# Kernel optimization log

Hardware: AMD Instinct MI355X
Metric: run time of the kernel (lower is better)

Reference implementation:

```python
import jax, jax.numpy as jnp
import numpy as np

N_NODES = 50000
E_DIM = 128
H_DIM = 256
OUT_DIM = 2
N_EDGES = 800000
NEG_SLOPE = 0.01  # nn.LeakyReLU default


def gcn_conv(x, W, b, src, dst, n):
    """PyG GCNConv: h = x @ W; add self-loops; sym-normalized scatter-add; + bias."""
    h = x @ W  # [N, H]
    loop = jnp.arange(n, dtype=src.dtype)
    s = jnp.concatenate([src, loop])
    d = jnp.concatenate([dst, loop])
    w = jnp.ones_like(s, dtype=h.dtype)
    deg = jax.ops.segment_sum(w, d, num_segments=n)  # in-degree incl. self-loop
    dis = jnp.where(deg > 0, jax.lax.rsqrt(deg), jnp.zeros_like(deg))
    norm = dis[s] * dis[d]  # [E+N]
    msg = h[s] * norm[:, None]  # gather + scale
    out = jax.ops.segment_sum(msg, d, num_segments=n)  # scatter-add to targets
    return out + b


def setup_inputs() -> dict:
    key = jax.random.key(0)
    ks = jax.random.split(key, 12)
    inp = {
        "mask_feature": jax.random.normal(ks[0], (N_NODES, E_DIM), jnp.float32),
        "feature": jax.random.normal(ks[1], (N_NODES, E_DIM), jnp.float32),
        "edge_index": jax.random.randint(ks[2], (2, N_EDGES), 0, N_NODES, jnp.int64 if jax.config.jax_enable_x64 else jnp.int32),
        "edge_type": jax.random.randint(ks[3], (N_EDGES,), 0, 2, jnp.int64 if jax.config.jax_enable_x64 else jnp.int32),
        # learned parameters
        "W_in": jax.random.normal(ks[4], (E_DIM, H_DIM), jnp.float32) * 0.05,
        "b_in": jnp.zeros((H_DIM,), jnp.float32),
        "Wg1": jax.random.normal(ks[5], (H_DIM, H_DIM), jnp.float32) * 0.05,
        "bg1": jnp.zeros((H_DIM,), jnp.float32),
        "Wg2": jax.random.normal(ks[6], (H_DIM, H_DIM), jnp.float32) * 0.05,
        "bg2": jnp.zeros((H_DIM,), jnp.float32),
        "W_out": jax.random.normal(ks[7], (H_DIM, OUT_DIM), jnp.float32) * 0.05,
        "b_out": jnp.zeros((OUT_DIM,), jnp.float32),
    }
    return inp


def reference(mask_feature, feature, edge_index, edge_type,
              W_in, b_in, Wg1, bg1, Wg2, bg2, W_out, b_out):
    src, dst = edge_index[0], edge_index[1]
    n = mask_feature.shape[0]
    # main branch
    x = jax.nn.leaky_relu(mask_feature @ W_in + b_in, NEG_SLOPE)
    x = gcn_conv(x, Wg1, bg1, src, dst, n)
    # dropout is identity at inference
    x = gcn_conv(x, Wg2, bg2, src, dst, n)
    x = x @ W_out + b_out  # [N, out_dim]
    # mask branch
    m = jax.nn.leaky_relu((feature - mask_feature) @ W_in + b_in, NEG_SLOPE)
    m = m @ W_out + b_out  # [N, out_dim]
    return x * m
```

## Files before the change

kernel.cpp:

```cpp
#include <hip/hip_runtime.h>


#define NEG_SLOPE 0.01f
constexpr int HD = 256;
constexpr int CHUNK = 4096;
constexpr int BSTRIDE = 8192;

typedef __bf16 bf16x8 __attribute__((ext_vector_type(8)));
typedef unsigned short u16x8 __attribute__((ext_vector_type(8)));
typedef float f32x4 __attribute__((ext_vector_type(4)));

#define MFMA16 __builtin_amdgcn_mfma_f32_16x16x32_bf16

__device__ inline void split1(float v, unsigned short& h, unsigned short& l) {
  unsigned u = __float_as_uint(v);
  unsigned hb = u & 0xFFFF0000u;
  float lf = v - __uint_as_float(hb);
  unsigned ul = __float_as_uint(lf);
  h = (unsigned short)(hb >> 16);
  l = (unsigned short)((ul + 0x7FFFu + ((ul >> 16) & 1u)) >> 16);
}

__device__ inline unsigned short bf16rne(float v) {
  unsigned u = __float_as_uint(v);
  return (unsigned short)((u + 0x7FFFu + ((u >> 16) & 1u)) >> 16);
}

__global__ __launch_bounds__(256) void k_prep(
    const float* __restrict__ Win, u16x8* __restrict__ Wf,
    const float* __restrict__ Wg1, const float* __restrict__ Wg2,
    const float* __restrict__ Wo, const float* __restrict__ bin,
    const float* __restrict__ bg1, const float* __restrict__ bg2,
    const float* __restrict__ bo, float4* __restrict__ E1,
    float2* __restrict__ E2, float* __restrict__ uv, int* __restrict__ cur) {
  __shared__ float wt[256][2];
  const int bid = blockIdx.x, tid = threadIdx.x;
  if (bid < 16) {
    int f = bid * 4 + (tid >> 6);
    int lane = tid & 63;
    int nt = f >> 2, ks = f & 3;
    int n = nt * 16 + (lane & 15);
    int k0 = ks * 32 + (lane >> 4) * 8;
    u16x8 outv;
    #pragma unroll
    for (int j = 0; j < 8; ++j)
      outv[j] = bf16rne(Win[(size_t)(k0 + j) * HD + n]);
    Wf[f * 64 + lane] = outv;
  } else if (bid == 16) {
    int r = tid;
    float s0 = 0.f, s1 = 0.f;
    for (int k = 0; k < 256; ++k) {
      float w = Wg2[r * 256 + k];
      s0 = fmaf(w, Wo[k * 2 + 0], s0);
      s1 = fmaf(w, Wo[k * 2 + 1], s1);
    }
    wt[r][0] = s0; wt[r][1] = s1;
    __syncthreads();
    float b0 = 0.f, b1 = 0.f;
    for (int k = 0; k < 256; ++k) {
      float w = Wg1[r * 256 + k];
      b0 = fmaf(w, wt[k][0], b0);
      b1 = fmaf(w, wt[k][1], b1);
    }
    E1[r] = make_float4(bin[r], b0, b1, 0.f);
    E2[r] = make_float2(Wo[r * 2 + 0], Wo[r * 2 + 1]);
    if (r < 2) {
      float u = 0.f, v = 0.f;
      for (int k = 0; k < 256; ++k) {
        u = fmaf(bg1[k], wt[k][r], u);
        v = fmaf(bg2[k], Wo[k * 2 + r], v);
      }
      uv[r] = u;
      uv[2 + r] = v + bo[r];
    }
  } else {
    cur[tid] = 0;
  }
}

__global__ __launch_bounds__(256) void k_scatter(
    const int* __restrict__ src, const int* __restrict__ dst,
    int* __restrict__ cur, unsigned* __restrict__ packed, int E) {
  __shared__ int bins[256], lstart[256], gbase[256], lcur[256];
  __shared__ int wsum[4];
  __shared__ unsigned sbuf[CHUNK];
  const int t = threadIdx.x, b = blockIdx.x;
  const int lane = t & 63, wid = t >> 6;
  bins[t] = 0;
  __syncthreads();
  const int e0 = b * CHUNK, e1 = min(e0 + CHUNK, E), m = e1 - e0;
  for (int e = e0 + t; e < e1; e += 256)
    atomicAdd(&bins[dst[e] >> 8], 1);
  __syncthreads();
  {
    int v = bins[t], incl = v;
    #pragma unroll
    for (int o = 1; o < 64; o <<= 1) {
      int tmp = __shfl_up(incl, o, 64);
      if (lane >= o) incl += tmp;
    }
    if (lane == 63) wsum[wid] = incl;
    __syncthreads();
    int woff = 0;
    for (int w = 0; w < wid; ++w) woff += wsum[w];
    int st = woff + incl - v;
    lstart[t] = st;
    lcur[t] = st;
    gbase[t] = v ? atomicAdd(&cur[t], v) : 0;
  }
  __syncthreads();
  for (int e = e0 + t; e < e1; e += 256) {
    int d = dst[e], s = src[e];
    int slot = atomicAdd(&lcur[d >> 8], 1);
    sbuf[slot] = ((unsigned)d << 16) | (unsigned)s;
  }
  __syncthreads();
  for (int i = t; i < m; i += 256) {
    unsigned pv = sbuf[i];
    int bin = pv >> 24;
    packed[(size_t)bin * BSTRIDE + gbase[bin] + (i - lstart[bin])] = pv;
  }
}

__global__ __launch_bounds__(256) void k_p2(
    const unsigned* __restrict__ packed, const int* __restrict__ cur,
    int* __restrict__ rp, float4* __restrict__ q, int* __restrict__ csr, int N) {
  __shared__ int cnt[256], sc[256];
  __shared__ int wsum[4];
  __shared__ unsigned short sbuf[BSTRIDE];
  const int t = threadIdx.x;
  const int B = blockIdx.x;
  const int lane = t & 63, wid = t >> 6;
  int tot = cur[t], incl = tot;
  #pragma unroll
  for (int o = 1; o < 64; o <<= 1) {
    int tmp = __shfl_up(incl, o, 64);
    if (lane >= o) incl += tmp;
  }
  if (lane == 63) wsum[wid] = incl;
  __syncthreads();
  int woff = 0;
  for (int w = 0; w < wid; ++w) woff += wsum[w];
  sc[t] = woff + incl - tot;
  __syncthreads();
  const int base = sc[B];
  const int ecnt = cur[B];
  const unsigned* pk = packed + (size_t)B * BSTRIDE;
  cnt[t] = 0;
  __syncthreads();
  for (int i = t; i < ecnt; i += 256)
    atomicAdd(&cnt[(pk[i] >> 16) & 0xFF], 1);
  __syncthreads();
  int v = cnt[t];
  incl = v;
  #pragma unroll
  for (int o = 1; o < 64; o <<= 1) {
    int tmp = __shfl_up(incl, o, 64);
    if (lane >= o) incl += tmp;
  }
  if (lane == 63) wsum[wid] = incl;
  __syncthreads();
  woff = 0;
  for (int w = 0; w < wid; ++w) woff += wsum[w];
  const int off = woff + incl - v;
  const int node = B * 256 + t;
  if (node < N) {
    rp[node] = base + off;
    ((float*)&q[node])[0] = rsqrtf((float)(v + 1));
  } else if (node == N) {
    rp[N] = base + off;
  }
  __syncthreads();
  cnt[t] = off;
  __syncthreads();
  for (int i = t; i < ecnt; i += 256) {
    unsigned pv = pk[i];
    int slot = atomicAdd(&cnt[(pv >> 16) & 0xFF], 1);
    sbuf[slot] = (unsigned short)(pv & 0xFFFFu);
  }
  __syncthreads();
  for (int i = t; i < ecnt; i += 256)
    csr[base + i] = (int)sbuf[i];
}

__global__ __launch_bounds__(64, 1) void k_gemm64(
    const float* __restrict__ mf, const float* __restrict__ fe,
    const u16x8* __restrict__ Wf, const float4* __restrict__ E1,
    const float2* __restrict__ E2, const float* __restrict__ bo,
    float4* __restrict__ q, float* __restrict__ Pm, int N) {
  const int lane = threadIdx.x;
  const int base = blockIdx.x * 16;
  int arow = base + (lane & 15);
  if (arow >= N) arow = N - 1;
  const int kb = (lane >> 4) * 8;
  const float* ap = mf + (size_t)arow * 128 + kb;
  const float* fp = fe + (size_t)arow * 128 + kb;

  bf16x8 Ah[4], Al[4], Kh[4], Kl[4];
  #pragma unroll
  for (int ks = 0; ks < 4; ++ks) {
    float x[8], y[8];
    *(float4*)&x[0] = *(const float4*)(ap + ks * 32);
    *(float4*)&x[4] = *(const float4*)(ap + ks * 32 + 4);
    *(float4*)&y[0] = *(const float4*)(fp + ks * 32);
    *(float4*)&y[4] = *(const float4*)(fp + ks * 32 + 4);
    u16x8 hA, lA, hM, lM;
    #pragma unroll
    for (int j = 0; j < 8; ++j) {
      unsigned short hh, ll;
      split1(x[j], hh, ll);        hA[j] = hh; lA[j] = ll;
      split1(y[j] - x[j], hh, ll); hM[j] = hh; lM[j] = ll;
    }
    Ah[ks] = __builtin_bit_cast(bf16x8, hA);
    Al[ks] = __builtin_bit_cast(bf16x8, lA);
    Kh[ks] = __builtin_bit_cast(bf16x8, hM);
    Kl[ks] = __builtin_bit_cast(bf16x8, lM);
  }

  const u16x8* wp = Wf + lane;
  float s0[4] = {}, s1[4] = {}, t0v[4] = {}, t1v[4] = {};
  u16x8 bA[4], bB[4];
  #pragma unroll
  for (int f = 0; f < 4; ++f) bA[f] = wp[f * 64];

  auto COMPUTE = [&](const u16x8* b, int nt) {
    f32x4 a0 = {0,0,0,0}, a1 = {0,0,0,0};
    f32x4 k0 = {0,0,0,0}, k1 = {0,0,0,0};
    #pragma unroll
    for (int ks = 0; ks < 4; ++ks) {
      bf16x8 bh = __builtin_bit_cast(bf16x8, b[ks]);
      a0 = MFMA16(Ah[ks], bh, a0, 0, 0, 0);
      a1 = MFMA16(Al[ks], bh, a1, 0, 0, 0);
      k0 = MFMA16(Kh[ks], bh, k0, 0, 0, 0);
      k1 = MFMA16(Kl[ks], bh, k1, 0, 0, 0);
    }
    const int col = nt * 16 + (lane & 15);
    const float4 e1 = E1[col];
    const float2 e2 = E2[col];
    #pragma unroll
    for (int r = 0; r < 4; ++r) {
      float a = (a0[r] + a1[r]) + e1.x;
      a = a > 0.f ? a : NEG_SLOPE * a;
      s0[r] = fmaf(a, e1.y, s0[r]); s1[r] = fmaf(a, e1.z, s1[r]);
      float m = (k0[r] + k1[r]) + e1.x;
      m = m > 0.f ? m : NEG_SLOPE * m;
      t0v[r] = fmaf(m, e2.x, t0v[r]); t1v[r] = fmaf(m, e2.y, t1v[r]);
    }
  };

  #pragma unroll 1
  for (int nt = 0; nt < 16; nt += 2) {
    #pragma unroll
    for (int f = 0; f < 4; ++f) bB[f] = wp[((nt + 1) * 4 + f) * 64];
    COMPUTE(bA, nt);
    if (nt + 2 < 16) {
      #pragma unroll
      for (int f = 0; f < 4; ++f) bA[f] = wp[((nt + 2) * 4 + f) * 64];
    }
    COMPUTE(bB, nt + 1);
  }

  #pragma unroll
  for (int o = 1; o < 16; o <<= 1) {
    #pragma unroll
    for (int r = 0; r < 4; ++r) {
      s0[r] += __shfl_xor(s0[r], o, 16);  s1[r] += __shfl_xor(s1[r], o, 16);
      t0v[r] += __shfl_xor(t0v[r], o, 16); t1v[r] += __shfl_xor(t1v[r], o, 16);
    }
  }
  if ((lane & 15) == 0) {
    float bo0 = bo[0], bo1 = bo[1];
    #pragma unroll
    for (int r = 0; r < 4; ++r) {
      int row = base + (lane >> 4) * 4 + r;
      if (row < N) {
        float* qf = (float*)&q[row];
        qf[1] = s0[r];
        qf[2] = s1[r];
        Pm[row * 2 + 0] = t0v[r] + bo0;
        Pm[row * 2 + 1] = t1v[r] + bo1;
      }
    }
  }
}

__global__ __launch_bounds__(256) void k_gather1(
    const int* __restrict__ rp, const int* __restrict__ csr,
    const float4* __restrict__ q, const float* __restrict__ uv,
    float* __restrict__ T2, int N) {
  int t = threadIdx.x;
  int n = blockIdx.x * 32 + (t >> 3);
  int l = t & 7;
  if (n >= N) return;
  int s0 = rp[n], s1 = rp[n + 1];
  float a0 = 0.f, a1 = 0.f;
  int j = s0 + l;
  for (; j + 8 < s1; j += 16) {
    int i0 = csr[j], i1 = csr[j + 8];
    float4 q0 = q[i0], q1 = q[i1];
    a0 = fmaf(q0.x, q0.y, a0); a1 = fmaf(q0.x, q0.z, a1);
    a0 = fmaf(q1.x, q1.y, a0); a1 = fmaf(q1.x, q1.z, a1);
  }
  if (j < s1) {
    float4 qa = q[csr[j]];
    a0 = fmaf(qa.x, qa.y, a0); a1 = fmaf(qa.x, qa.z, a1);
  }
  a0 += __shfl_xor(a0, 1, 8); a1 += __shfl_xor(a1, 1, 8);
  a0 += __shfl_xor(a0, 2, 8); a1 += __shfl_xor(a1, 2, 8);
  a0 += __shfl_xor(a0, 4, 8); a1 += __shfl_xor(a1, 4, 8);
  if (l == 0) {
    float4 qn = q[n];
    float d = qn.x;
    T2[n * 2 + 0] = d * (d * fmaf(d, qn.y, a0) + uv[0]);
    T2[n * 2 + 1] = d * (d * fmaf(d, qn.z, a1) + uv[1]);
  }
}

__global__ __launch_bounds__(256) void k_gather2(
    const int* __restrict__ rp, const int* __restrict__ csr,
    const float* __restrict__ T2, const float4* __restrict__ q,
    const float* __restrict__ uv, const float* __restrict__ Pm,
    float* __restrict__ out, int N) {
  int t = threadIdx.x;
  int n = blockIdx.x * 32 + (t >> 3);
  int l = t & 7;
  if (n >= N) return;
  int s0 = rp[n], s1 = rp[n + 1];
  float a0 = 0.f, a1 = 0.f;
  int j = s0 + l;
  for (; j + 8 < s1; j += 16) {
    int i0 = csr[j], i1 = csr[j + 8];
    float2 v0 = *(const float2*)&T2[i0 * 2];
    float2 v1 = *(const float2*)&T2[i1 * 2];
    a0 += v0.x + v1.x; a1 += v0.y + v1.y;
  }
  if (j < s1) {
    float2 va = *(const float2*)&T2[csr[j] * 2];
    a0 += va.x; a1 += va.y;
  }
  a0 += __shfl_xor(a0, 1, 8); a1 += __shfl_xor(a1, 1, 8);
  a0 += __shfl_xor(a0, 2, 8); a1 += __shfl_xor(a1, 2, 8);
  a0 += __shfl_xor(a0, 4, 8); a1 += __shfl_xor(a1, 4, 8);
  if (l == 0) {
    float d = q[n].x;
    float2 tv = *(const float2*)&T2[n * 2];
    float z0 = d * (tv.x + a0) + uv[2];
    float z1 = d * (tv.y + a1) + uv[3];
    out[n * 2 + 0] = z0 * Pm[n * 2 + 0];
    out[n * 2 + 1] = z1 * Pm[n * 2 + 1];
  }
}

extern "C" void kernel_launch(void* const* d_in, const int* in_sizes, int n_in,
                              void* d_out, int out_size, void* d_ws, size_t ws_size,
                              hipStream_t stream) {
  const float* mf  = (const float*)d_in[0];
  const float* fe  = (const float*)d_in[1];
  const int*   ei  = (const int*)d_in[2];
  const float* Win = (const float*)d_in[4];
  const float* bin = (const float*)d_in[5];
  const float* Wg1 = (const float*)d_in[6];
  const float* bg1 = (const float*)d_in[7];
  const float* Wg2 = (const float*)d_in[8];
  const float* bg2 = (const float*)d_in[9];
  const float* Wo  = (const float*)d_in[10];
  const float* bo  = (const float*)d_in[11];
  float* out = (float*)d_out;

  const int ED = 128;
  const int N = in_sizes[0] / ED;
  const int E = in_sizes[3];
  const int* src = ei;
  const int* dst = ei + E;

  char* ws = (char*)d_ws;
  size_t off = 0;
  auto carve = [&](size_t bytes) {
    char* p = ws + off;
    off += (bytes + 255) & ~(size_t)255;
    return p;
  };
  int*      cur    = (int*)carve(256 * 4);
  unsigned* packed = (unsigned*)carve((size_t)256 * BSTRIDE * 4);
  int*      csr    = (int*)carve((size_t)E * 4);
  int*      rp     = (int*)carve((size_t)(N + 1) * 4);
  float4*   q      = (float4*)carve((size_t)N * 16);
  float*    T2     = (float*)carve((size_t)N * 2 * 4);
  float*    Pm     = (float*)carve((size_t)N * 2 * 4);
  float4*   E1     = (float4*)carve((size_t)HD * 16);
  float2*   E2     = (float2*)carve((size_t)HD * 8);
  float*    uv     = (float*)carve(4 * 4);
  u16x8*    Wf     = (u16x8*)carve((size_t)64 * 64 * 16);
  (void)ws_size; (void)n_in; (void)out_size;

  const int NB  = (E + CHUNK - 1) / CHUNK;
  const int NP2 = (N + 255) / 256;
  const int Gg  = (N + 15) / 16;
  const int Gt  = (N + 31) / 32;

  k_prep<<<18, 256, 0, stream>>>(Win, Wf, Wg1, Wg2, Wo, bin, bg1, bg2, bo,
                                 E1, E2, uv, cur);
  k_scatter<<<NB, 256, 0, stream>>>(src, dst, cur, packed, E);
  k_p2<<<NP2, 256, 0, stream>>>(packed, cur, rp, q, csr, N);
  k_gemm64<<<Gg, 64, 0, stream>>>(mf, fe, Wf, E1, E2, bo, q, Pm, N);
  k_gather1<<<Gt, 256, 0, stream>>>(rp, csr, q, uv, T2, N);
  k_gather2<<<Gt, 256, 0, stream>>>(rp, csr, T2, q, uv, Pm, out, N);
}
```

Before: 95.38 us.

## Fuse GEMM and edge-scatter kernels into one launch with block-range dispatch

Merges the dense projection kernel and the edge bucketing scatter into a single kernel. The first Gg blocks do the GEMM and the rest do the scatter, so the compute-bound MFMA work and the memory- and atomic-bound bucketing can run at the same time, and one launch is removed. GEMM blocks now hold four waves covering 64 rows and stage the E1/E2 epilogue vectors in shared memory. The LDS buffer is sized for the scatter path, which may limit occupancy of GEMM blocks. The GEMM also now runs before k_p2, which is safe only because the two kernels write disjoint fields of q.

```diff
diff --git a/kernel.cpp b/kernel.cpp
--- a/kernel.cpp
+++ b/kernel.cpp
@@ -78,14 +78,129 @@
   }
 }
 
-__global__ __launch_bounds__(256) void k_scatter(
+__global__ __launch_bounds__(256, 2) void k_main(
+    const float* __restrict__ mf, const float* __restrict__ fe,
+    const u16x8* __restrict__ Wf, const float4* __restrict__ E1,
+    const float2* __restrict__ E2, const float* __restrict__ bo,
+    float4* __restrict__ q, float* __restrict__ Pm,
     const int* __restrict__ src, const int* __restrict__ dst,
-    int* __restrict__ cur, unsigned* __restrict__ packed, int E) {
-  __shared__ int bins[256], lstart[256], gbase[256], lcur[256];
-  __shared__ int wsum[4];
-  __shared__ unsigned sbuf[CHUNK];
-  const int t = threadIdx.x, b = blockIdx.x;
-  const int lane = t & 63, wid = t >> 6;
+    int* __restrict__ cur, unsigned* __restrict__ packed,
+    int N, int E, int Gg) {
+  __shared__ __align__(16) char smem[20608];
+  const int tid = threadIdx.x;
+  const int lane = tid & 63, wid = tid >> 6;
+
+  if ((int)blockIdx.x < Gg) {
+    float4* sE1 = (float4*)smem;
+    float2* sE2 = (float2*)(smem + 4096);
+    sE1[tid] = E1[tid];
+    sE2[tid] = E2[tid];
+
+    const int gb = blockIdx.x * 64;
+    const int base = gb + wid * 16;
+    int arow = base + (lane & 15);
+    if (arow >= N) arow = N - 1;
+    const int kb = (lane >> 4) * 8;
+    const float* ap = mf + (size_t)arow * 128 + kb;
+    const float* fp = fe + (size_t)arow * 128 + kb;
+
+    bf16x8 Ah[4], Al[4], Kh[4], Kl[4];
+    #pragma unroll
+    for (int ks = 0; ks < 4; ++ks) {
+      float x[8], y[8];
+      *(float4*)&x[0] = *(const float4*)(ap + ks * 32);
+      *(float4*)&x[4] = *(const float4*)(ap + ks * 32 + 4);
+      *(float4*)&y[0] = *(const float4*)(fp + ks * 32);
+      *(float4*)&y[4] = *(const float4*)(fp + ks * 32 + 4);
+      u16x8 hA, lA, hM, lM;
+      #pragma unroll
+      for (int j = 0; j < 8; ++j) {
+        unsigned short hh, ll;
+        split1(x[j], hh, ll);        hA[j] = hh; lA[j] = ll;
+        split1(y[j] - x[j], hh, ll); hM[j] = hh; lM[j] = ll;
+      }
+      Ah[ks] = __builtin_bit_cast(bf16x8, hA);
+      Al[ks] = __builtin_bit_cast(bf16x8, lA);
+      Kh[ks] = __builtin_bit_cast(bf16x8, hM);
+      Kl[ks] = __builtin_bit_cast(bf16x8, lM);
+    }
+    __syncthreads();
+
+    const u16x8* wp = Wf + lane;
+    float s0[4] = {}, s1[4] = {}, t0v[4] = {}, t1v[4] = {};
+    u16x8 bA[4], bB[4];
+    #pragma unroll
+    for (int f = 0; f < 4; ++f) bA[f] = wp[f * 64];
+
+    auto COMPUTE = [&](const u16x8* b, int nt) {
+      f32x4 a0 = {0,0,0,0}, a1 = {0,0,0,0};
+      f32x4 k0 = {0,0,0,0}, k1 = {0,0,0,0};
+      #pragma unroll
+      for (int ks = 0; ks < 4; ++ks) {
+        bf16x8 bh = __builtin_bit_cast(bf16x8, b[ks]);
+        a0 = MFMA16(Ah[ks], bh, a0, 0, 0, 0);
+        a1 = MFMA16(Al[ks], bh, a1, 0, 0, 0);
+        k0 = MFMA16(Kh[ks], bh, k0, 0, 0, 0);
+        k1 = MFMA16(Kl[ks], bh, k1, 0, 0, 0);
+      }
+      const int col = nt * 16 + (lane & 15);
+      const float4 e1 = sE1[col];
+      const float2 e2 = sE2[col];
+      #pragma unroll
+      for (int r = 0; r < 4; ++r) {
+        float a = (a0[r] + a1[r]) + e1.x;
+        a = a > 0.f ? a : NEG_SLOPE * a;
+        s0[r] = fmaf(a, e1.y, s0[r]); s1[r] = fmaf(a, e1.z, s1[r]);
+        float m = (k0[r] + k1[r]) + e1.x;
+        m = m > 0.f ? m : NEG_SLOPE * m;
+        t0v[r] = fmaf(m, e2.x, t0v[r]); t1v[r] = fmaf(m, e2.y, t1v[r]);
+      }
+    };
+
+    #pragma unroll 1
+    for (int nt = 0; nt < 16; nt += 2) {
+      #pragma unroll
+      for (int f = 0; f < 4; ++f) bB[f] = wp[((nt + 1) * 4 + f) * 64];
+      COMPUTE(bA, nt);
+      if (nt + 2 < 16) {
+        #pragma unroll
+        for (int f = 0; f < 4; ++f) bA[f] = wp[((nt + 2) * 4 + f) * 64];
+      }
+      COMPUTE(bB, nt + 1);
+    }
+
+    #pragma unroll
+    for (int o = 1; o < 16; o <<= 1) {
+      #pragma unroll
+      for (int r = 0; r < 4; ++r) {
+        s0[r] += __shfl_xor(s0[r], o, 16);  s1[r] += __shfl_xor(s1[r], o, 16);
+        t0v[r] += __shfl_xor(t0v[r], o, 16); t1v[r] += __shfl_xor(t1v[r], o, 16);
+      }
+    }
+    if ((lane & 15) == 0) {
+      float bo0 = bo[0], bo1 = bo[1];
+      #pragma unroll
+      for (int r = 0; r < 4; ++r) {
+        int row = base + (lane >> 4) * 4 + r;
+        if (row < N) {
+          float* qf = (float*)&q[row];
+          qf[1] = s0[r];
+          qf[2] = s1[r];
+          Pm[row * 2 + 0] = t0v[r] + bo0;
+          Pm[row * 2 + 1] = t1v[r] + bo1;
+        }
+      }
+    }
+    return;
+  }
+
+  int* bins   = (int*)smem;
+  int* lstart = (int*)(smem + 1024);
+  int* gbase  = (int*)(smem + 2048);
+  int* lcur   = (int*)(smem + 3072);
+  int* wsum   = (int*)(smem + 4096);
+  unsigned* sbuf = (unsigned*)(smem + 4112);
+  const int t = tid, b = blockIdx.x - Gg;
   bins[t] = 0;
   __syncthreads();
   const int e0 = b * CHUNK, e1 = min(e0 + CHUNK, E), m = e1 - e0;
@@ -181,107 +296,6 @@
   __syncthreads();
   for (int i = t; i < ecnt; i += 256)
     csr[base + i] = (int)sbuf[i];
-}
-
-__global__ __launch_bounds__(64, 1) void k_gemm64(
-    const float* __restrict__ mf, const float* __restrict__ fe,
-    const u16x8* __restrict__ Wf, const float4* __restrict__ E1,
-    const float2* __restrict__ E2, const float* __restrict__ bo,
-    float4* __restrict__ q, float* __restrict__ Pm, int N) {
-  const int lane = threadIdx.x;
-  const int base = blockIdx.x * 16;
-  int arow = base + (lane & 15);
-  if (arow >= N) arow = N - 1;
-  const int kb = (lane >> 4) * 8;
-  const float* ap = mf + (size_t)arow * 128 + kb;
-  const float* fp = fe + (size_t)arow * 128 + kb;
-
-  bf16x8 Ah[4], Al[4], Kh[4], Kl[4];
-  #pragma unroll
-  for (int ks = 0; ks < 4; ++ks) {
-    float x[8], y[8];
-    *(float4*)&x[0] = *(const float4*)(ap + ks * 32);
-    *(float4*)&x[4] = *(const float4*)(ap + ks * 32 + 4);
-    *(float4*)&y[0] = *(const float4*)(fp + ks * 32);
-    *(float4*)&y[4] = *(const float4*)(fp + ks * 32 + 4);
-    u16x8 hA, lA, hM, lM;
-    #pragma unroll
-    for (int j = 0; j < 8; ++j) {
-      unsigned short hh, ll;
-      split1(x[j], hh, ll);        hA[j] = hh; lA[j] = ll;
-      split1(y[j] - x[j], hh, ll); hM[j] = hh; lM[j] = ll;
-    }
-    Ah[ks] = __builtin_bit_cast(bf16x8, hA);
-    Al[ks] = __builtin_bit_cast(bf16x8, lA);
-    Kh[ks] = __builtin_bit_cast(bf16x8, hM);
-    Kl[ks] = __builtin_bit_cast(bf16x8, lM);
-  }
-
-  const u16x8* wp = Wf + lane;
-  float s0[4] = {}, s1[4] = {}, t0v[4] = {}, t1v[4] = {};
-  u16x8 bA[4], bB[4];
-  #pragma unroll
-  for (int f = 0; f < 4; ++f) bA[f] = wp[f * 64];
-
-  auto COMPUTE = [&](const u16x8* b, int nt) {
-    f32x4 a0 = {0,0,0,0}, a1 = {0,0,0,0};
-    f32x4 k0 = {0,0,0,0}, k1 = {0,0,0,0};
-    #pragma unroll
-    for (int ks = 0; ks < 4; ++ks) {
-      bf16x8 bh = __builtin_bit_cast(bf16x8, b[ks]);
-      a0 = MFMA16(Ah[ks], bh, a0, 0, 0, 0);
-      a1 = MFMA16(Al[ks], bh, a1, 0, 0, 0);
-      k0 = MFMA16(Kh[ks], bh, k0, 0, 0, 0);
-      k1 = MFMA16(Kl[ks], bh, k1, 0, 0, 0);
-    }
-    const int col = nt * 16 + (lane & 15);
-    const float4 e1 = E1[col];
-    const float2 e2 = E2[col];
-    #pragma unroll
-    for (int r = 0; r < 4; ++r) {
-      float a = (a0[r] + a1[r]) + e1.x;
-      a = a > 0.f ? a : NEG_SLOPE * a;
-      s0[r] = fmaf(a, e1.y, s0[r]); s1[r] = fmaf(a, e1.z, s1[r]);
-      float m = (k0[r] + k1[r]) + e1.x;
-      m = m > 0.f ? m : NEG_SLOPE * m;
-      t0v[r] = fmaf(m, e2.x, t0v[r]); t1v[r] = fmaf(m, e2.y, t1v[r]);
-    }
-  };
-
-  #pragma unroll 1
-  for (int nt = 0; nt < 16; nt += 2) {
-    #pragma unroll
-    for (int f = 0; f < 4; ++f) bB[f] = wp[((nt + 1) * 4 + f) * 64];
-    COMPUTE(bA, nt);
-    if (nt + 2 < 16) {
-      #pragma unroll
-      for (int f = 0; f < 4; ++f) bA[f] = wp[((nt + 2) * 4 + f) * 64];
-    }
-    COMPUTE(bB, nt + 1);
-  }
-
-  #pragma unroll
-  for (int o = 1; o < 16; o <<= 1) {
-    #pragma unroll
-    for (int r = 0; r < 4; ++r) {
-      s0[r] += __shfl_xor(s0[r], o, 16);  s1[r] += __shfl_xor(s1[r], o, 16);
-      t0v[r] += __shfl_xor(t0v[r], o, 16); t1v[r] += __shfl_xor(t1v[r], o, 16);
-    }
-  }
-  if ((lane & 15) == 0) {
-    float bo0 = bo[0], bo1 = bo[1];
-    #pragma unroll
-    for (int r = 0; r < 4; ++r) {
-      int row = base + (lane >> 4) * 4 + r;
-      if (row < N) {
-        float* qf = (float*)&q[row];
-        qf[1] = s0[r];
-        qf[2] = s1[r];
-        Pm[row * 2 + 0] = t0v[r] + bo0;
-        Pm[row * 2 + 1] = t1v[r] + bo1;
-      }
-    }
-  }
 }
 
 __global__ __launch_bounds__(256) void k_gather1(
@@ -395,14 +409,14 @@
 
   const int NB  = (E + CHUNK - 1) / CHUNK;
   const int NP2 = (N + 255) / 256;
-  const int Gg  = (N + 15) / 16;
+  const int Gg  = (N + 63) / 64;
   const int Gt  = (N + 31) / 32;
 
   k_prep<<<18, 256, 0, stream>>>(Win, Wf, Wg1, Wg2, Wo, bin, bg1, bg2, bo,
                                  E1, E2, uv, cur);
-  k_scatter<<<NB, 256, 0, stream>>>(src, dst, cur, packed, E);
+  k_main<<<Gg + NB, 256, 0, stream>>>(mf, fe, Wf, E1, E2, bo, q, Pm,
+                                      src, dst, cur, packed, N, E, Gg);
   k_p2<<<NP2, 256, 0, stream>>>(packed, cur, rp, q, csr, N);
-  k_gemm64<<<Gg, 64, 0, stream>>>(mf, fe, Wf, E1, E2, bo, q, Pm, N);
   k_gather1<<<Gt, 256, 0, stream>>>(rp, csr, q, uv, T2, N);
   k_gather2<<<Gt, 256, 0, stream>>>(rp, csr, T2, q, uv, Pm, out, N);
 }
```

Result: faster. 82.65 us (median of 2 runs) (-13.3%).
